# Kernel optimization log

Hardware: AMD Instinct MI355X
Metric: run time of the kernel (lower is better)

## Reference

```python
import jax, jax.numpy as jnp
import numpy as np

NUM_FEAT = 1024
NUM_GROUP = 16
DIM_K = NUM_FEAT // NUM_GROUP  # 64
FEAT_DIM = 64
WAVE_LENGTH = 1000.0


def position_embedding(box, ctx_box):
    # box: (M,4), ctx_box: (N,4) corner encoding -> (M*N, 64)
    xmin, ymin, xmax, ymax = jnp.split(box, 4, axis=1)            # (M,1) each
    bw = xmax - xmin + 1.0
    bh = ymax - ymin + 1.0
    cx = 0.5 * (xmin + xmax)
    cy = 0.5 * (ymin + ymax)
    cxmin, cymin, cxmax, cymax = jnp.split(ctx_box, 4, axis=1)    # (N,1) each
    cbw = cxmax - cxmin + 1.0
    cbh = cymax - cymin + 1.0
    ccx = 0.5 * (cxmin + cxmax)
    ccy = 0.5 * (cymin + cymax)
    dx = jnp.log(jnp.clip(jnp.abs((cx - ccx.T) / bw), 1e-3))      # (M,N)
    dy = jnp.log(jnp.clip(jnp.abs((cy - ccy.T) / bh), 1e-3))
    dw = jnp.log(cbw.T / bw)
    dh = jnp.log(cbh.T / bh)
    pos = jnp.stack((dx, dy, dw, dh), axis=2)                     # (M,N,4)
    feat_range = jnp.arange(FEAT_DIM // 8, dtype=jnp.float32)     # (8,)
    dim_mat = jnp.power(jnp.float32(WAVE_LENGTH), (8.0 / FEAT_DIM) * feat_range)
    div = (100.0 * pos)[..., None] / dim_mat                      # (M,N,4,8)
    emb = jnp.concatenate((jnp.sin(div), jnp.cos(div)), axis=3)   # (M,N,4,16)
    M, N = pos.shape[0], pos.shape[1]
    return emb.reshape(M * N, FEAT_DIM)


def setup_inputs() -> dict:
    key = jax.random.key(0)
    ks = jax.random.split(key, 12)
    M, N = 512, 1024

    def make_boxes(k, n):
        k1, k2 = jax.random.split(k)
        xy = jax.random.uniform(k1, (n, 2), dtype=jnp.float32) * 800.0
        wh = jax.random.uniform(k2, (n, 2), dtype=jnp.float32) * 200.0 + 1.0
        return jnp.concatenate([xy, xy + wh], axis=1)             # valid corners

    return {
        "feat": jax.random.normal(ks[0], (M, NUM_FEAT), dtype=jnp.float32),
        "ctx_feat": jax.random.normal(ks[1], (N, NUM_FEAT), dtype=jnp.float32),
        "box": make_boxes(ks[2], M),
        "ctx_box": make_boxes(ks[3], N),
        # torch Linear stores weight as (out, in); apply as x @ W.T + b
        "w_fc_gt": jax.random.normal(ks[4], (NUM_FEAT, 1024), dtype=jnp.float32) * 0.01,
        "b_fc_gt": jnp.zeros((NUM_FEAT,), dtype=jnp.float32),
        "w_fc_ctx": jax.random.normal(ks[5], (NUM_FEAT, 1024), dtype=jnp.float32) * 0.01,
        "b_fc_ctx": jnp.zeros((NUM_FEAT,), dtype=jnp.float32),
        "w_pos_gt": jax.random.normal(ks[6], (NUM_GROUP, FEAT_DIM), dtype=jnp.float32) * 0.01,
        "b_pos_gt": jnp.zeros((NUM_GROUP,), dtype=jnp.float32),
        "w_pos_ctx": jax.random.normal(ks[7], (NUM_GROUP, FEAT_DIM), dtype=jnp.float32) * 0.01,
        "b_pos_ctx": jnp.zeros((NUM_GROUP,), dtype=jnp.float32),
        # grouped 1x1 conv (16384 -> 1024, groups=16): per-group weight (64 out, 1024 in)
        "w_conv": jax.random.normal(ks[8], (NUM_GROUP, DIM_K, NUM_FEAT), dtype=jnp.float32) * 0.02,
        "b_conv": jnp.zeros((NUM_FEAT,), dtype=jnp.float32),
    }


def reference(feat, ctx_feat, box, ctx_box,
              w_fc_gt, b_fc_gt, w_fc_ctx, b_fc_ctx,
              w_pos_gt, b_pos_gt, w_pos_ctx, b_pos_ctx,
              w_conv, b_conv):
    M, N = feat.shape[0], ctx_feat.shape[0]
    # positional bias per group: (M*N,64) -relu-> linear -> (G,M,N)
    pe_gt = jax.nn.relu(position_embedding(box, ctx_box))
    pos_gt = (pe_gt @ w_pos_gt.T + b_pos_gt).T.reshape(NUM_GROUP, M, N)
    pe_ctx = jax.nn.relu(position_embedding(ctx_box, box))
    pos_ctx = (pe_ctx @ w_pos_ctx.T + b_pos_ctx).T.reshape(NUM_GROUP, N, M)
    # grouped projections
    q = (feat @ w_fc_gt.T + b_fc_gt).reshape(M, NUM_GROUP, DIM_K)
    k = (ctx_feat @ w_fc_ctx.T + b_fc_ctx).reshape(N, NUM_GROUP, DIM_K)
    scores = jnp.einsum('mgd,ngd->gmn', q, k) / np.float32(np.sqrt(DIM_K))  # (G,M,N)
    # gt <- ctx attention with log-position bias
    w1 = jax.nn.softmax(jnp.log(jnp.clip(pos_gt, 1e-6)) + scores, axis=-1)  # (G,M,N)
    att1 = jnp.einsum('gmn,nc->mgc', w1, ctx_feat)                          # (M,G,1024)
    out_gt = jnp.einsum('mgc,goc->mgo', att1, w_conv).reshape(M, NUM_FEAT) + b_conv
    # ctx <- gt attention (note: original module reuses gt_ctx_linear_out here)
    w2 = jax.nn.softmax(jnp.log(jnp.clip(pos_ctx, 1e-6)) + scores.transpose(0, 2, 1), axis=-1)  # (G,N,M)
    att2 = jnp.einsum('gnm,mc->ngc', w2, feat)                              # (N,G,1024)
    out_ctx = jnp.einsum('ngc,goc->ngo', att2, w_conv).reshape(N, NUM_FEAT) + b_conv
    return out_gt, out_ctx
```

## Files before the change

kernel.cpp:

```cpp
#include <hip/hip_runtime.h>
#include <math.h>


typedef __attribute__((ext_vector_type(8))) short short8;
typedef __attribute__((ext_vector_type(4))) float floatx4;
typedef __attribute__((ext_vector_type(4))) _Float16 half4;

__device__ inline unsigned short f32_bf16_rne(float x) {
    union { float f; unsigned u; } v; v.f = x;
    unsigned u = v.u;
    return (unsigned short)((u + 0x7fffu + ((u >> 16) & 1u)) >> 16);
}

__device__ inline float bf16_f32(unsigned short h) {
    union { unsigned u; float f; } v; v.u = (unsigned)h << 16;
    return v.f;
}

__device__ __forceinline__ floatx4 mfma16(short8 a, short8 b, floatx4 c) {
    return __builtin_amdgcn_mfma_f32_16x16x32_bf16(a, b, c, 0, 0, 0);
}

__device__ __forceinline__ void gemm_tile_bf16(
    const unsigned short* __restrict__ Ab, int lda,
    const unsigned short* __restrict__ Bb, int ldb, int K,
    unsigned short* __restrict__ Cb, int ldc,
    const float* __restrict__ biasvec,
    unsigned short* As, unsigned short* Bs)
{
    const int tid = threadIdx.x;
    const int lr = tid >> 2;
    const int lk = (tid & 3) * 8;
    const int lane = tid & 63;
    const int wave = tid >> 6;
    const int qr = (wave >> 1) * 32;
    const int qc = (wave & 1) * 32;
    const int m = lane & 15;
    const int quad = lane >> 4;

    const unsigned short* Ap = Ab + (long long)lr * lda + lk;
    const unsigned short* Bp = Bb + (long long)lr * ldb + lk;
    unsigned short* AsW = As + lr * 72 + lk;
    unsigned short* BsW = Bs + lr * 72 + lk;
    const unsigned short* a0p = As + (qr + m) * 72 + quad * 8;
    const unsigned short* b0p = Bs + (qc + m) * 72 + quad * 8;

    floatx4 acc00 = {0.f,0.f,0.f,0.f}, acc01 = {0.f,0.f,0.f,0.f};
    floatx4 acc10 = {0.f,0.f,0.f,0.f}, acc11 = {0.f,0.f,0.f,0.f};

    int4 pa0 = *(const int4*)Ap;
    int4 pa1 = *(const int4*)(Ap + 32);
    int4 pb0 = *(const int4*)Bp;
    int4 pb1 = *(const int4*)(Bp + 32);

    for (int k0 = 0; ; ) {
        __syncthreads();
        *(int4*)AsW        = pa0;
        *(int4*)(AsW + 32) = pa1;
        *(int4*)BsW        = pb0;
        *(int4*)(BsW + 32) = pb1;
        __syncthreads();
        const int kn = k0 + 64;
        if (kn < K) {
            pa0 = *(const int4*)(Ap + kn);
            pa1 = *(const int4*)(Ap + kn + 32);
            pb0 = *(const int4*)(Bp + kn);
            pb1 = *(const int4*)(Bp + kn + 32);
        }
        #pragma unroll
        for (int kk = 0; kk < 64; kk += 32) {
            short8 a0 = *(const short8*)(a0p + kk);
            short8 a1 = *(const short8*)(a0p + 16 * 72 + kk);
            short8 b0 = *(const short8*)(b0p + kk);
            short8 b1 = *(const short8*)(b0p + 16 * 72 + kk);
            acc00 = mfma16(a0, b0, acc00);
            acc01 = mfma16(a0, b1, acc01);
            acc10 = mfma16(a1, b0, acc10);
            acc11 = mfma16(a1, b1, acc11);
        }
        k0 = kn;
        if (k0 >= K) break;
    }

    float bias0 = 0.f, bias1 = 0.f;
    if (biasvec) { bias0 = biasvec[qc + m]; bias1 = biasvec[qc + 16 + m]; }

    const floatx4 accs[2][2] = { {acc00, acc01}, {acc10, acc11} };
    #pragma unroll
    for (int i = 0; i < 2; ++i)
        #pragma unroll
        for (int r = 0; r < 4; ++r) {
            const int lrow = qr + i * 16 + quad * 4 + r;
            #pragma unroll
            for (int j = 0; j < 2; ++j) {
                const int lcol = qc + j * 16 + m;
                float val = accs[i][j][r] + (j ? bias1 : bias0);
                Cb[(long long)lrow * ldc + lcol] = f32_bf16_rne(val);
            }
        }
}

__global__ __launch_bounds__(256) void projvt_kernel(
    const unsigned short* __restrict__ in_bf, const unsigned short* __restrict__ wgt,
    const unsigned short* __restrict__ wctx,
    const float* __restrict__ bgt, const float* __restrict__ bctx,
    unsigned short* __restrict__ qk,
    const unsigned short* __restrict__ wconv, unsigned short* __restrict__ vt)
{
    __shared__ __align__(16) unsigned short As[64 * 72];
    __shared__ __align__(16) unsigned short Bs[64 * 72];
    if (blockIdx.z == 0) {
        const int bm = blockIdx.x * 64, bn = blockIdx.y * 64;
        const unsigned short* B = (bm < 512) ? wgt : wctx;
        const float* bias = (bm < 512) ? bgt : bctx;
        gemm_tile_bf16(in_bf + (long long)bm * 1024, 1024,
                       B + (long long)bn * 1024, 1024, 1024,
                       qk + (long long)bm * 1024 + bn, 1024,
                       bias + bn, As, Bs);
    } else {
        const int g = blockIdx.y;
        const int bn = blockIdx.x * 64;
        gemm_tile_bf16(wconv + (long long)g * 65536, 1024,
                       in_bf + (long long)bn * 1024, 1024, 1024,
                       vt + (long long)g * 98304 + bn, 1536,
                       nullptr, As, Bs);
    }
}

__global__ __launch_bounds__(256) void pos_bias_kernel(
    const float* __restrict__ box, const float* __restrict__ ctx_box,
    const float* __restrict__ w_gt, const float* __restrict__ b_gt,
    const float* __restrict__ w_ctx, const float* __restrict__ b_ctx,
    _Float16* __restrict__ bias_gt, _Float16* __restrict__ bias_ctx)
{
    const bool first = (blockIdx.z == 0);
    const float* boxA = first ? box : ctx_box;
    const float* boxB = first ? ctx_box : box;
    const float* w_pos = first ? w_gt : w_ctx;
    const float* b_pos = first ? b_gt : b_ctx;
    _Float16* out = first ? bias_gt : bias_ctx;
    const int shift = first ? 10 : 9;

    __shared__ __align__(16) unsigned short AsH[64 * 72];
    __shared__ __align__(16) unsigned short AsL[64 * 72];
    __shared__ __align__(16) unsigned short BsH[16 * 72];
    __shared__ __align__(16) unsigned short BsL[16 * 72];

    const int tid = threadIdx.x;

    {
        const int g = tid >> 4;
        const int d = (tid & 15) * 4;
        float4 wv = *(const float4*)(w_pos + g * 64 + d);
        ushort4 h, l;
        h.x = f32_bf16_rne(wv.x); l.x = f32_bf16_rne(wv.x - bf16_f32(h.x));
        h.y = f32_bf16_rne(wv.y); l.y = f32_bf16_rne(wv.y - bf16_f32(h.y));
        h.z = f32_bf16_rne(wv.z); l.z = f32_bf16_rne(wv.z - bf16_f32(h.z));
        h.w = f32_bf16_rne(wv.w); l.w = f32_bf16_rne(wv.w - bf16_f32(h.w));
        *(ushort4*)&BsH[g * 72 + d] = h;
        *(ushort4*)&BsL[g * 72 + d] = l;
    }

    const long long pbase = (long long)blockIdx.x * 64;
    {
        const int pl = tid & 63;
        const int p = tid >> 6;
        const long long pair = pbase + pl;
        const int i = (int)(pair >> shift);
        const int j = (int)(pair & ((1 << shift) - 1));
        float4 ba = *(const float4*)(boxA + i * 4);
        float4 bb = *(const float4*)(boxB + j * 4);
        float posv;
        if (p == 0) {
            float bw = ba.z - ba.x + 1.f;
            float cx = 0.5f * (ba.x + ba.z), ccx = 0.5f * (bb.x + bb.z);
            posv = __logf(fmaxf(fabsf((cx - ccx) / bw), 1e-3f));
        } else if (p == 1) {
            float bh = ba.w - ba.y + 1.f;
            float cy = 0.5f * (ba.y + ba.w), ccy = 0.5f * (bb.y + bb.w);
            posv = __logf(fmaxf(fabsf((cy - ccy) / bh), 1e-3f));
        } else if (p == 2) {
            float bw = ba.z - ba.x + 1.f, cbw = bb.z - bb.x + 1.f;
            posv = __logf(cbw / bw);
        } else {
            float bh = ba.w - ba.y + 1.f, cbh = bb.w - bb.y + 1.f;
            posv = __logf(cbh / bh);
        }
        const float w100[8] = {100.f, 42.169650342f, 17.782794100f, 7.498942093f,
                               3.162277660f, 1.333521432f, 0.562341325f, 0.237137371f};
        short8 sh, sl, ch, cl;
        #pragma unroll
        for (int f = 0; f < 8; ++f) {
            float s, c;
            __sincosf(posv * w100[f], &s, &c);
            s = fmaxf(s, 0.f);
            c = fmaxf(c, 0.f);
            unsigned short hs = f32_bf16_rne(s);
            unsigned short hc = f32_bf16_rne(c);
            sh[f] = (short)hs; sl[f] = (short)f32_bf16_rne(s - bf16_f32(hs));
            ch[f] = (short)hc; cl[f] = (short)f32_bf16_rne(c - bf16_f32(hc));
        }
        *(short8*)&AsH[pl * 72 + p * 16]     = sh;
        *(short8*)&AsH[pl * 72 + p * 16 + 8] = ch;
        *(short8*)&AsL[pl * 72 + p * 16]     = sl;
        *(short8*)&AsL[pl * 72 + p * 16 + 8] = cl;
    }
    __syncthreads();

    const int lane = tid & 63;
    const int w = tid >> 6;
    const int m = lane & 15;
    const int quad = lane >> 4;
    const unsigned short* apH = &AsH[(w * 16 + m) * 72 + quad * 8];
    const unsigned short* apL = &AsL[(w * 16 + m) * 72 + quad * 8];
    const unsigned short* bpH = &BsH[m * 72 + quad * 8];
    const unsigned short* bpL = &BsL[m * 72 + quad * 8];
    floatx4 acc = {0.f, 0.f, 0.f, 0.f};
    acc = mfma16(*(const short8*)apH,        *(const short8*)bpH,        acc);
    acc = mfma16(*(const short8*)(apH + 32), *(const short8*)(bpH + 32), acc);
    acc = mfma16(*(const short8*)apH,        *(const short8*)bpL,        acc);
    acc = mfma16(*(const short8*)(apH + 32), *(const short8*)(bpL + 32), acc);
    acc = mfma16(*(const short8*)apL,        *(const short8*)bpH,        acc);
    acc = mfma16(*(const short8*)(apL + 32), *(const short8*)(bpH + 32), acc);

    const float bpv = b_pos[m];
    half4 o;
    #pragma unroll
    for (int r = 0; r < 4; ++r)
        o[r] = (_Float16)__logf(fmaxf(acc[r] + bpv, 1e-6f));
    *(half4*)(out + (long long)m * 524288 + pbase + w * 16 + quad * 4) = o;
}

template <int NC>
__device__ __forceinline__ void attn_body(
    int g, int bx,
    const unsigned short* __restrict__ qA, const unsigned short* __restrict__ qB,
    const _Float16* __restrict__ bias, const unsigned short* __restrict__ vt,
    int vt_colbase, const float* __restrict__ b_conv, float* __restrict__ outp,
    unsigned short* tile, unsigned short* wpack, float* redA, float* redB)
{
    constexpr int NCOL = NC * 64;
    constexpr int WS = NCOL + 8;

    const int bm = bx * 16;
    const int tid = threadIdx.x;
    const int lane = tid & 63;
    const int w = tid >> 6;
    const int m = lane & 15;
    const int quad = lane >> 4;
    const int lr = tid >> 2;
    const int lk = (tid & 3) * 8;

    const _Float16* bias_g = bias + (long long)g * 524288
                           + (long long)(bm + quad * 4) * NCOL + w * 16 + m;

    const unsigned short* ap = qA + (long long)(bm + m) * 1024 + g * 64 + quad * 8;
    short8 aq0 = *(const short8*)ap;
    short8 aq1 = *(const short8*)(ap + 32);

    const unsigned short* Bp = qB + (long long)lr * 1024 + g * 64 + lk;
    unsigned short* tW = tile + lr * 72 + lk;
    const unsigned short* bq = tile + (w * 16 + m) * 72 + quad * 8;

    float v[NC][4];

    int4 pk0 = *(const int4*)Bp;
    int4 pk1 = *(const int4*)(Bp + 32);

    #pragma unroll
    for (int c = 0; c < NC; ++c) {
        __syncthreads();
        *(int4*)tW        = pk0;
        *(int4*)(tW + 32) = pk1;
        __syncthreads();
        if (c + 1 < NC) {
            const unsigned short* nb = Bp + (long long)(c + 1) * 64 * 1024;
            pk0 = *(const int4*)nb;
            pk1 = *(const int4*)(nb + 32);
        }
        float bv[4];
        #pragma unroll
        for (int r = 0; r < 4; ++r)
            bv[r] = (float)bias_g[(long long)r * NCOL + c * 64];
        short8 kb0 = *(const short8*)bq;
        short8 kb1 = *(const short8*)(bq + 32);
        floatx4 acc = {0.f, 0.f, 0.f, 0.f};
        acc = mfma16(aq0, kb0, acc);
        acc = mfma16(aq1, kb1, acc);
        #pragma unroll
        for (int r = 0; r < 4; ++r)
            v[c][r] = fmaf(0.125f, acc[r], bv[r]);
    }

    const unsigned short* Vp = vt + (long long)g * 98304 + (long long)lr * 1536
                             + vt_colbase + lk;
    int4 pv0 = *(const int4*)Vp;
    int4 pv1 = *(const int4*)(Vp + 32);

    float rmax[4];
    #pragma unroll
    for (int r = 0; r < 4; ++r) {
        float mx = v[0][r];
        #pragma unroll
        for (int c = 1; c < NC; ++c) mx = fmaxf(mx, v[c][r]);
        #pragma unroll
        for (int off = 1; off < 16; off <<= 1)
            mx = fmaxf(mx, __shfl_xor(mx, off, 64));
        rmax[r] = mx;
    }
    if (m == 0) {
        #pragma unroll
        for (int r = 0; r < 4; ++r) redA[w * 16 + quad * 4 + r] = rmax[r];
    }
    __syncthreads();
    #pragma unroll
    for (int r = 0; r < 4; ++r)
        rmax[r] = fmaxf(fmaxf(redA[quad*4+r], redA[16 + quad*4+r]),
                        fmaxf(redA[32 + quad*4+r], redA[48 + quad*4+r]));

    float rsum[4] = {0.f, 0.f, 0.f, 0.f};
    #pragma unroll
    for (int c = 0; c < NC; ++c)
        #pragma unroll
        for (int r = 0; r < 4; ++r) {
            v[c][r] = __expf(v[c][r] - rmax[r]);
            rsum[r] += v[c][r];
        }
    #pragma unroll
    for (int r = 0; r < 4; ++r)
        #pragma unroll
        for (int off = 1; off < 16; off <<= 1)
            rsum[r] += __shfl_xor(rsum[r], off, 64);
    if (m == 0) {
        #pragma unroll
        for (int r = 0; r < 4; ++r) redB[w * 16 + quad * 4 + r] = rsum[r];
    }
    __syncthreads();
    float rinv[4];
    #pragma unroll
    for (int r = 0; r < 4; ++r)
        rinv[r] = 1.f / (redB[quad*4+r] + redB[16 + quad*4+r] +
                         redB[32 + quad*4+r] + redB[48 + quad*4+r]);

    #pragma unroll
    for (int c = 0; c < NC; ++c)
        #pragma unroll
        for (int r = 0; r < 4; ++r)
            wpack[(quad * 4 + r) * WS + c * 64 + w * 16 + m] =
                f32_bf16_rne(v[c][r] * rinv[r]);

    floatx4 oacc = {0.f, 0.f, 0.f, 0.f};
    const unsigned short* awp = wpack + m * WS + quad * 8;
    #pragma unroll
    for (int kc = 0; kc < NC; ++kc) {
        __syncthreads();
        *(int4*)tW        = pv0;
        *(int4*)(tW + 32) = pv1;
        __syncthreads();
        if (kc + 1 < NC) {
            const unsigned short* nv = Vp + (kc + 1) * 64;
            pv0 = *(const int4*)nv;
            pv1 = *(const int4*)(nv + 32);
        }
        short8 a0 = *(const short8*)(awp + kc * 64);
        short8 a1 = *(const short8*)(awp + kc * 64 + 32);
        short8 b0 = *(const short8*)bq;
        short8 b1 = *(const short8*)(bq + 32);
        oacc = mfma16(a0, b0, oacc);
        oacc = mfma16(a1, b1, oacc);
    }

    const int o = w * 16 + m;
    const float bc = b_conv[g * 64 + o];
    #pragma unroll
    for (int r = 0; r < 4; ++r)
        outp[(long long)(bm + quad * 4 + r) * 1024 + g * 64 + o] = oacc[r] + bc;
}

__global__ __launch_bounds__(256) void attn_out_kernel(
    const unsigned short* __restrict__ qk,
    const _Float16* __restrict__ bias_gt, const _Float16* __restrict__ bias_ctx,
    const unsigned short* __restrict__ vt, const float* __restrict__ b_conv,
    float* __restrict__ out_gt, float* __restrict__ out_ctx)
{
    __shared__ __align__(16) unsigned short tile[64 * 72];
    __shared__ __align__(16) unsigned short wpack[16 * 1032];
    __shared__ float redA[64], redB[64];

    const int z = blockIdx.z;
    if (z < 16) {
        if (blockIdx.x >= 32) return;
        attn_body<16>(z, blockIdx.x, qk, qk + 524288LL, bias_gt, vt, 512,
                      b_conv, out_gt, tile, wpack, redA, redB);
    } else {
        attn_body<8>(z - 16, blockIdx.x, qk + 524288LL, qk, bias_ctx, vt, 0,
                     b_conv, out_ctx, tile, wpack, redA, redB);
    }
}

__global__ __launch_bounds__(256) void conv5_f32_bf16(
    const float* s0, unsigned short* d0, int n0,
    const float* s1, unsigned short* d1, int n1,
    const float* s2, unsigned short* d2, int n2,
    const float* s3, unsigned short* d3, int n3,
    const float* s4, unsigned short* d4, int n4)
{
    const float* s; unsigned short* d; int n;
    switch (blockIdx.y) {
        case 0: s = s0; d = d0; n = n0; break;
        case 1: s = s1; d = d1; n = n1; break;
        case 2: s = s2; d = d2; n = n2; break;
        case 3: s = s3; d = d3; n = n3; break;
        default: s = s4; d = d4; n = n4; break;
    }
    int idx = (blockIdx.x * 256 + threadIdx.x) * 4;
    if (idx < n) {
        float4 v = *(const float4*)(s + idx);
        ushort4 o;
        o.x = f32_bf16_rne(v.x); o.y = f32_bf16_rne(v.y);
        o.z = f32_bf16_rne(v.z); o.w = f32_bf16_rne(v.w);
        *(ushort4*)(d + idx) = o;
    }
}

extern "C" void kernel_launch(void* const* d_in, const int* in_sizes, int n_in,
                              void* d_out, int out_size, void* d_ws, size_t ws_size,
                              hipStream_t stream)
{
    const float* feat     = (const float*)d_in[0];
    const float* ctx_feat = (const float*)d_in[1];
    const float* box      = (const float*)d_in[2];
    const float* ctx_box  = (const float*)d_in[3];
    const float* w_fc_gt  = (const float*)d_in[4];
    const float* b_fc_gt  = (const float*)d_in[5];
    const float* w_fc_ctx = (const float*)d_in[6];
    const float* b_fc_ctx = (const float*)d_in[7];
    const float* w_pos_gt = (const float*)d_in[8];
    const float* b_pos_gt = (const float*)d_in[9];
    const float* w_pos_ctx= (const float*)d_in[10];
    const float* b_pos_ctx= (const float*)d_in[11];
    const float* w_conv   = (const float*)d_in[12];
    const float* b_conv   = (const float*)d_in[13];

    float* ws = (float*)d_ws;
    unsigned short* in_bf   = (unsigned short*)ws;
    unsigned short* ctx_bf  = in_bf + 524288LL;
    unsigned short* qk_bf   = in_bf + 1572864LL;
    _Float16* bias_gt  = (_Float16*)(ws + 1572864LL);
    _Float16* bias_ctx = (_Float16*)(ws + 5767168LL);
    unsigned short* wconv_bf = (unsigned short*)(ws + 9961472LL);
    unsigned short* vt_bf    = (unsigned short*)(ws + 10485760LL);
    unsigned short* wfcgt_bf = (unsigned short*)(ws + 11272192LL);
    unsigned short* wfcctx_bf= wfcgt_bf + 1048576LL;

    float* out_gt  = (float*)d_out;
    float* out_ctx = (float*)d_out + 524288LL;

    hipLaunchKernelGGL(conv5_f32_bf16, dim3(1024, 5), dim3(256), 0, stream,
                       feat, in_bf, 524288,
                       ctx_feat, ctx_bf, 1048576,
                       w_fc_gt, wfcgt_bf, 1048576,
                       w_fc_ctx, wfcctx_bf, 1048576,
                       w_conv, wconv_bf, 1048576);

    hipLaunchKernelGGL(pos_bias_kernel, dim3(8192, 1, 2), dim3(256), 0, stream,
                       box, ctx_box, w_pos_gt, b_pos_gt, w_pos_ctx, b_pos_ctx,
                       bias_gt, bias_ctx);

    hipLaunchKernelGGL(projvt_kernel, dim3(24, 16, 2), dim3(256), 0, stream,
                       in_bf, wfcgt_bf, wfcctx_bf, b_fc_gt, b_fc_ctx, qk_bf,
                       wconv_bf, vt_bf);

    hipLaunchKernelGGL(attn_out_kernel, dim3(64, 1, 32), dim3(256), 0, stream,
                       qk_bf, bias_gt, bias_ctx, vt_bf, b_conv, out_gt, out_ctx);
}
```

Before: 171.0 us.

## Load attention K/V operands straight from global and deepen GEMM prefetch

The attention kernel no longer stages K and V tiles through shared memory with two barriers per chunk. Each lane now loads its MFMA B-operand fragments directly from global memory into registers and prefetches the next chunk one step ahead, which removes many __syncthreads and the LDS tile. Separately, the tiled GEMM now prefetches two K-steps ahead in registers to hide more global latency, at the cost of extra registers. The direct loads are less coalesced (16-byte pieces spread across rows) and may lean on cache bandwidth instead of LDS.

```diff
diff --git a/kernel.cpp b/kernel.cpp
--- a/kernel.cpp
+++ b/kernel.cpp
@@ -52,6 +52,10 @@
     int4 pa1 = *(const int4*)(Ap + 32);
     int4 pb0 = *(const int4*)Bp;
     int4 pb1 = *(const int4*)(Bp + 32);
+    int4 qa0 = *(const int4*)(Ap + 64);
+    int4 qa1 = *(const int4*)(Ap + 96);
+    int4 qb0 = *(const int4*)(Bp + 64);
+    int4 qb1 = *(const int4*)(Bp + 96);
 
     for (int k0 = 0; ; ) {
         __syncthreads();
@@ -60,12 +64,13 @@
         *(int4*)BsW        = pb0;
         *(int4*)(BsW + 32) = pb1;
         __syncthreads();
-        const int kn = k0 + 64;
-        if (kn < K) {
-            pa0 = *(const int4*)(Ap + kn);
-            pa1 = *(const int4*)(Ap + kn + 32);
-            pb0 = *(const int4*)(Bp + kn);
-            pb1 = *(const int4*)(Bp + kn + 32);
+        pa0 = qa0; pa1 = qa1; pb0 = qb0; pb1 = qb1;
+        const int kf = k0 + 128;
+        if (kf < K) {
+            qa0 = *(const int4*)(Ap + kf);
+            qa1 = *(const int4*)(Ap + kf + 32);
+            qb0 = *(const int4*)(Bp + kf);
+            qb1 = *(const int4*)(Bp + kf + 32);
         }
         #pragma unroll
         for (int kk = 0; kk < 64; kk += 32) {
@@ -78,7 +83,7 @@
             acc10 = mfma16(a1, b0, acc10);
             acc11 = mfma16(a1, b1, acc11);
         }
-        k0 = kn;
+        k0 += 64;
         if (k0 >= K) break;
     }
 
@@ -237,7 +242,7 @@
     const unsigned short* __restrict__ qA, const unsigned short* __restrict__ qB,
     const _Float16* __restrict__ bias, const unsigned short* __restrict__ vt,
     int vt_colbase, const float* __restrict__ b_conv, float* __restrict__ outp,
-    unsigned short* tile, unsigned short* wpack, float* redA, float* redB)
+    unsigned short* wpack, float* redA, float* redB)
 {
     constexpr int NCOL = NC * 64;
     constexpr int WS = NCOL + 8;
@@ -248,8 +253,6 @@
     const int w = tid >> 6;
     const int m = lane & 15;
     const int quad = lane >> 4;
-    const int lr = tid >> 2;
-    const int lk = (tid & 3) * 8;
 
     const _Float16* bias_g = bias + (long long)g * 524288
                            + (long long)(bm + quad * 4) * NCOL + w * 16 + m;
@@ -258,44 +261,32 @@
     short8 aq0 = *(const short8*)ap;
     short8 aq1 = *(const short8*)(ap + 32);
 
-    const unsigned short* Bp = qB + (long long)lr * 1024 + g * 64 + lk;
-    unsigned short* tW = tile + lr * 72 + lk;
-    const unsigned short* bq = tile + (w * 16 + m) * 72 + quad * 8;
+    const unsigned short* bbase = qB + (long long)(w * 16 + m) * 1024 + g * 64 + quad * 8;
 
     float v[NC][4];
-
-    int4 pk0 = *(const int4*)Bp;
-    int4 pk1 = *(const int4*)(Bp + 32);
+    short8 b0 = *(const short8*)bbase;
+    short8 b1 = *(const short8*)(bbase + 32);
 
     #pragma unroll
     for (int c = 0; c < NC; ++c) {
-        __syncthreads();
-        *(int4*)tW        = pk0;
-        *(int4*)(tW + 32) = pk1;
-        __syncthreads();
+        short8 nb0, nb1;
         if (c + 1 < NC) {
-            const unsigned short* nb = Bp + (long long)(c + 1) * 64 * 1024;
-            pk0 = *(const int4*)nb;
-            pk1 = *(const int4*)(nb + 32);
+            const unsigned short* nb = bbase + (long long)(c + 1) * 65536;
+            nb0 = *(const short8*)nb;
+            nb1 = *(const short8*)(nb + 32);
         }
         float bv[4];
         #pragma unroll
         for (int r = 0; r < 4; ++r)
             bv[r] = (float)bias_g[(long long)r * NCOL + c * 64];
-        short8 kb0 = *(const short8*)bq;
-        short8 kb1 = *(const short8*)(bq + 32);
         floatx4 acc = {0.f, 0.f, 0.f, 0.f};
-        acc = mfma16(aq0, kb0, acc);
-        acc = mfma16(aq1, kb1, acc);
+        acc = mfma16(aq0, b0, acc);
+        acc = mfma16(aq1, b1, acc);
         #pragma unroll
         for (int r = 0; r < 4; ++r)
             v[c][r] = fmaf(0.125f, acc[r], bv[r]);
-    }
-
-    const unsigned short* Vp = vt + (long long)g * 98304 + (long long)lr * 1536
-                             + vt_colbase + lk;
-    int4 pv0 = *(const int4*)Vp;
-    int4 pv1 = *(const int4*)(Vp + 32);
+        b0 = nb0; b1 = nb1;
+    }
 
     float rmax[4];
     #pragma unroll
@@ -349,25 +340,28 @@
             wpack[(quad * 4 + r) * WS + c * 64 + w * 16 + m] =
                 f32_bf16_rne(v[c][r] * rinv[r]);
 
+    const unsigned short* vbase = vt + (long long)g * 98304
+                                + (long long)(w * 16 + m) * 1536 + vt_colbase + quad * 8;
+    short8 vb0 = *(const short8*)vbase;
+    short8 vb1 = *(const short8*)(vbase + 32);
+
+    __syncthreads();
+
     floatx4 oacc = {0.f, 0.f, 0.f, 0.f};
     const unsigned short* awp = wpack + m * WS + quad * 8;
     #pragma unroll
     for (int kc = 0; kc < NC; ++kc) {
-        __syncthreads();
-        *(int4*)tW        = pv0;
-        *(int4*)(tW + 32) = pv1;
-        __syncthreads();
+        short8 nv0, nv1;
         if (kc + 1 < NC) {
-            const unsigned short* nv = Vp + (kc + 1) * 64;
-            pv0 = *(const int4*)nv;
-            pv1 = *(const int4*)(nv + 32);
+            const unsigned short* nv = vbase + (kc + 1) * 64;
+            nv0 = *(const short8*)nv;
+            nv1 = *(const short8*)(nv + 32);
         }
         short8 a0 = *(const short8*)(awp + kc * 64);
         short8 a1 = *(const short8*)(awp + kc * 64 + 32);
-        short8 b0 = *(const short8*)bq;
-        short8 b1 = *(const short8*)(bq + 32);
-        oacc = mfma16(a0, b0, oacc);
-        oacc = mfma16(a1, b1, oacc);
+        oacc = mfma16(a0, vb0, oacc);
+        oacc = mfma16(a1, vb1, oacc);
+        vb0 = nv0; vb1 = nv1;
     }
 
     const int o = w * 16 + m;
@@ -383,7 +377,6 @@
     const unsigned short* __restrict__ vt, const float* __restrict__ b_conv,
     float* __restrict__ out_gt, float* __restrict__ out_ctx)
 {
-    __shared__ __align__(16) unsigned short tile[64 * 72];
     __shared__ __align__(16) unsigned short wpack[16 * 1032];
     __shared__ float redA[64], redB[64];
 
@@ -391,10 +384,10 @@
     if (z < 16) {
         if (blockIdx.x >= 32) return;
         attn_body<16>(z, blockIdx.x, qk, qk + 524288LL, bias_gt, vt, 512,
-                      b_conv, out_gt, tile, wpack, redA, redB);
+                      b_conv, out_gt, wpack, redA, redB);
     } else {
         attn_body<8>(z - 16, blockIdx.x, qk + 524288LL, qk, bias_ctx, vt, 0,
-                     b_conv, out_ctx, tile, wpack, redA, redB);
+                     b_conv, out_ctx, wpack, redA, redB);
     }
 }
 
```

Result: slower. 180.1 us (+5.4%).
